# Performance work log

Measured on AMD Instinct MI355X. Metric: run time of the kernel, lower is better.

Reference implementation:

```python
import jax, jax.numpy as jnp
import numpy as np
import math

MODEL_DIM = 64
HEAD_DIM = 16


def setup_inputs() -> dict:
    key = jax.random.key(0)
    ks = jax.random.split(key, 9)
    B, T = 4, 4096
    idx = jax.random.normal(ks[0], (B, T, MODEL_DIM), dtype=jnp.float32)
    s_in = 1.0 / math.sqrt(MODEL_DIM)
    s_h = 1.0 / math.sqrt(HEAD_DIM)
    return {
        "idx": idx,
        "Wk": jax.random.normal(ks[1], (HEAD_DIM, MODEL_DIM), dtype=jnp.float32) * s_in,
        "bk": jax.random.normal(ks[2], (HEAD_DIM,), dtype=jnp.float32) * 0.02,
        "Wq": jax.random.normal(ks[3], (HEAD_DIM, MODEL_DIM), dtype=jnp.float32) * s_in,
        "bq": jax.random.normal(ks[4], (HEAD_DIM,), dtype=jnp.float32) * 0.02,
        "Wv": jax.random.normal(ks[5], (HEAD_DIM, MODEL_DIM), dtype=jnp.float32) * s_in,
        "bv": jax.random.normal(ks[6], (HEAD_DIM,), dtype=jnp.float32) * 0.02,
        "Wp": jax.random.normal(ks[7], (MODEL_DIM, HEAD_DIM), dtype=jnp.float32) * s_h,
        "bp": jax.random.normal(ks[8], (MODEL_DIM,), dtype=jnp.float32) * 0.02,
    }


def reference(idx, Wk, bk, Wq, bq, Wv, bv, Wp, bp):
    # idx: [B, T, model_dim]
    k = idx @ Wk.T + bk  # [B, T, H]
    q = idx @ Wq.T + bq
    v = idx @ Wv.T + bv
    scale = 1.0 / math.sqrt(HEAD_DIM)
    att = jnp.einsum("bth,bsh->bts", q, k) * scale  # [B, T, T]
    att = jnp.tril(att)
    # faithful to masked_fill(attention == 0, -inf): any exact-zero entry
    # (upper triangle after tril, plus accidental zeros) becomes -inf
    att = jnp.where(att == 0, -jnp.inf, att)
    att = jax.nn.softmax(att, axis=-1)
    av = jnp.einsum("bts,bsh->bth", att, v)  # [B, T, H]
    return av @ Wp.T + bp  # [B, T, model_dim]
```

## Files before the change

kernel.cpp:

```cpp
#include <hip/hip_runtime.h>
#include <hip/hip_bf16.h>
#include <stdint.h>

#define DEV __device__ __forceinline__

typedef short s4v __attribute__((ext_vector_type(4)));
typedef float f4v __attribute__((ext_vector_type(4)));

static constexpr int T = 4096;
static constexpr int BATCH = 4;
static constexpr int MD = 64;
static constexpr int H = 16;
static constexpr int PB = T * H;

#if __has_builtin(__builtin_amdgcn_mfma_f32_16x16x16bf16_1k)
DEV f4v mfma16(s4v a, s4v b, f4v c) {
    return __builtin_amdgcn_mfma_f32_16x16x16bf16_1k(a, b, c, 0, 0, 0);
}
#elif __has_builtin(__builtin_amdgcn_mfma_f32_16x16x16_bf16)
typedef __bf16 bf4v __attribute__((ext_vector_type(4)));
DEV f4v mfma16(s4v a, s4v b, f4v c) {
    return __builtin_amdgcn_mfma_f32_16x16x16_bf16(__builtin_bit_cast(bf4v, a),
                                                   __builtin_bit_cast(bf4v, b), c, 0, 0, 0);
}
#else
DEV f4v mfma16(s4v a, s4v b, f4v c) {
    asm("v_mfma_f32_16x16x16_bf16 %0, %1, %2, %0" : "+v"(c) : "v"(a), "v"(b));
    return c;
}
#endif

DEV short f2bf(float x) {
    uint32_t u = __builtin_bit_cast(uint32_t, x);
    u += 0x7fffu + ((u >> 16) & 1u);
    return (short)(u >> 16);
}

DEV float ex2(float x) {
#if __has_builtin(__builtin_amdgcn_exp2f)
    return __builtin_amdgcn_exp2f(x);
#else
    return exp2f(x);
#endif
}

__global__ __launch_bounds__(256) void k_proj(
    const float* __restrict__ idx,
    const float* __restrict__ Wk, const float* __restrict__ bk,
    const float* __restrict__ Wq, const float* __restrict__ bq,
    const float* __restrict__ Wv, const float* __restrict__ bv,
    short* __restrict__ qp, short* __restrict__ kp, short* __restrict__ vp)
{
    const int w = threadIdx.x >> 6, lane = threadIdx.x & 63;
    const int a = lane & 15, g = lane >> 4;
    const int tile = blockIdx.x * 4 + w;
    const int b = tile >> 8;
    const int trow0 = (tile & 255) << 4;

    const float* rb = idx + (size_t)(b * T + trow0) * MD;

    s4v xf[4], wqf[4], wkf[4], wvf[4];
#pragma unroll
    for (int kc = 0; kc < 4; ++kc) {
        const int ko = kc * 16 + 4 * g;
        f4v x = *(const f4v*)(rb + a * MD + ko);
        f4v q = *(const f4v*)(Wq + a * MD + ko);
        f4v k = *(const f4v*)(Wk + a * MD + ko);
        f4v v = *(const f4v*)(Wv + a * MD + ko);
        xf[kc]  = s4v{f2bf(x.x), f2bf(x.y), f2bf(x.z), f2bf(x.w)};
        wqf[kc] = s4v{f2bf(q.x), f2bf(q.y), f2bf(q.z), f2bf(q.w)};
        wkf[kc] = s4v{f2bf(k.x), f2bf(k.y), f2bf(k.z), f2bf(k.w)};
        wvf[kc] = s4v{f2bf(v.x), f2bf(v.y), f2bf(v.z), f2bf(v.w)};
    }
    f4v aq = {0.f,0.f,0.f,0.f}, ak = {0.f,0.f,0.f,0.f}, av = {0.f,0.f,0.f,0.f};
#pragma unroll
    for (int kc = 0; kc < 4; ++kc) {
        aq = mfma16(wqf[kc], xf[kc], aq);
        ak = mfma16(wkf[kc], xf[kc], ak);
        av = mfma16(xf[kc], wvf[kc], av);
    }
    const int slot = b * PB + (tile & 255) * 256 + g * 64 + a * 4;
    f4v bqv = *(const f4v*)(bq + 4 * g);
    f4v bkv = *(const f4v*)(bk + 4 * g);
    const float bvs = bv[a];
    const float CS = 0.36067376022224085f;
    *(s4v*)(qp + slot) = s4v{f2bf((aq.x + bqv.x) * CS), f2bf((aq.y + bqv.y) * CS),
                             f2bf((aq.z + bqv.z) * CS), f2bf((aq.w + bqv.w) * CS)};
    *(s4v*)(kp + slot) = s4v{f2bf(ak.x + bkv.x), f2bf(ak.y + bkv.y),
                             f2bf(ak.z + bkv.z), f2bf(ak.w + bkv.w)};
    *(s4v*)(vp + slot) = s4v{f2bf(av.x + bvs), f2bf(av.y + bvs),
                             f2bf(av.z + bvs), f2bf(av.w + bvs)};
}

DEV void proc_range(int lo, int hi, s4v Qf, int tq, int g,
                    const short* __restrict__ kb, const short* __restrict__ vb,
                    f4v& acc, float& lp)
{
    int st = lo;
    for (; st + 4 <= hi; st += 4) {
        s4v Kf[4], Vf[4];
#pragma unroll
        for (int u = 0; u < 4; ++u) {
            Kf[u] = *(const s4v*)(kb + (st + u) * 256);
            Vf[u] = *(const s4v*)(vb + (st + u) * 256);
        }
#pragma unroll
        for (int u = 0; u < 4; ++u) {
            f4v S = mfma16(Kf[u], Qf, f4v{0.f,0.f,0.f,0.f});
            const int sb = (st + u) * 16 + 4 * g;
            f4v p;
#pragma unroll
            for (int r = 0; r < 4; ++r) {
                const float e = ex2(S[r]);
                p[r] = (sb + r <= tq) ? e : 0.f;
            }
            lp += p.x + p.y + p.z + p.w;
            const s4v Pf = s4v{f2bf(p.x), f2bf(p.y), f2bf(p.z), f2bf(p.w)};
            acc = mfma16(Pf, Vf[u], acc);
        }
    }
    for (; st < hi; ++st) {
        s4v Kf = *(const s4v*)(kb + st * 256);
        s4v Vf = *(const s4v*)(vb + st * 256);
        f4v S = mfma16(Kf, Qf, f4v{0.f,0.f,0.f,0.f});
        const int sb = st * 16 + 4 * g;
        f4v p;
#pragma unroll
        for (int r = 0; r < 4; ++r) {
            const float e = ex2(S[r]);
            p[r] = (sb + r <= tq) ? e : 0.f;
        }
        lp += p.x + p.y + p.z + p.w;
        const s4v Pf = s4v{f2bf(p.x), f2bf(p.y), f2bf(p.z), f2bf(p.w)};
        acc = mfma16(Pf, Vf, acc);
    }
}

__global__ __launch_bounds__(256) void k_fused(
    const short* __restrict__ qp, const short* __restrict__ kp,
    const short* __restrict__ vp,
    const float* __restrict__ Wp, const float* __restrict__ bp,
    float* __restrict__ out)
{
    const int bx = blockIdx.x;
    const int b = bx >> 7, j = bx & 127;
    const int tid = threadIdx.x;
    const int w = tid >> 6, lane = tid & 63;
    const int a = lane & 15, g = lane >> 4;

    const int qtA = j, qtB = 255 - j;
    const int ntA = j + 1;
    const int ntot = 257;

    const short* qb = qp + b * PB;
    const short* kb = kp + b * PB + g * 64 + a * 4;
    const short* vb = vp + b * PB + g * 64 + a * 4;

    const s4v QfA = *(const s4v*)(qb + qtA * 256 + g * 64 + a * 4);
    const s4v QfB = *(const s4v*)(qb + qtB * 256 + g * 64 + a * 4);
    const int tqA = qtA * 16 + a, tqB = qtB * 16 + a;

    const int vLo = min(w * 65, ntot);
    const int vHi = min(vLo + 65, ntot);

    f4v accA = {0.f,0.f,0.f,0.f}, accB = {0.f,0.f,0.f,0.f};
    float lpA = 0.f, lpB = 0.f;

    proc_range(vLo, min(vHi, ntA), QfA, tqA, g, kb, vb, accA, lpA);
    proc_range(max(vLo - ntA, 0), vHi - ntA, QfB, tqB, g, kb, vb, accB, lpB);

    __shared__ float pacc[8 * 64 * 4];
    __shared__ float plp[8 * 16];

    *(f4v*)&pacc[((w * 2 + 0) * 64 + lane) * 4] = accA;
    *(f4v*)&pacc[((w * 2 + 1) * 64 + lane) * 4] = accB;

    float lA = lpA + __shfl_xor(lpA, 16); lA += __shfl_xor(lA, 32);
    float lB = lpB + __shfl_xor(lpB, 16); lB += __shfl_xor(lB, 32);
    if (lane < 16) {
        plp[(w * 2 + 0) * 16 + lane] = lA;
        plp[(w * 2 + 1) * 16 + lane] = lB;
    }
    __syncthreads();

    if (tid < 128) {
        const int X = tid >> 6, i = (tid >> 2) & 15, dc = tid & 3;
        float av[16];
#pragma unroll
        for (int h = 0; h < 16; ++h) av[h] = 0.f;
        float l = 0.f;
#pragma unroll
        for (int ww = 0; ww < 4; ++ww) {
            const int base = ((ww * 2 + X) * 64 + (i >> 2) * 16) * 4 + (i & 3);
#pragma unroll
            for (int h = 0; h < 16; ++h) av[h] += pacc[base + h * 4];
            l += plp[(ww * 2 + X) * 16 + i];
        }
        const float inv = 1.f / l;
        const int qt = X ? qtB : qtA;

        float* orow = out + ((size_t)(b * T) + qt * 16 + i) * 64 + dc * 16;
#pragma unroll
        for (int j4 = 0; j4 < 4; ++j4) {
            f4v o;
#pragma unroll
            for (int jj = 0; jj < 4; ++jj) {
                const int d = dc * 16 + j4 * 4 + jj;
                const float* wr = Wp + d * 16;
                float s = 0.f;
#pragma unroll
                for (int h = 0; h < 16; ++h) s += av[h] * wr[h];
                o[jj] = bp[d] + s * inv;
            }
            *(f4v*)(orow + j4 * 4) = o;
        }
    }
}

extern "C" void kernel_launch(void* const* d_in, const int* in_sizes, int n_in,
                              void* d_out, int out_size, void* d_ws, size_t ws_size,
                              hipStream_t stream) {
    const float* idx = (const float*)d_in[0];
    const float* Wk  = (const float*)d_in[1];
    const float* bk  = (const float*)d_in[2];
    const float* Wq  = (const float*)d_in[3];
    const float* bq  = (const float*)d_in[4];
    const float* Wv  = (const float*)d_in[5];
    const float* bv  = (const float*)d_in[6];
    const float* Wp  = (const float*)d_in[7];
    const float* bp  = (const float*)d_in[8];
    float* out = (float*)d_out;

    short* qp = (short*)d_ws;
    short* kp = qp + BATCH * PB;
    short* vp = kp + BATCH * PB;

    k_proj<<<256, 256, 0, stream>>>(idx, Wk, bk, Wq, bq, Wv, bv, qp, kp, vp);
    k_fused<<<512, 256, 0, stream>>>(qp, kp, vp, Wp, bp, out);
}
```

Measured before the change: 31.37 us.

## Double-buffer K/V register loads in groups of eight and mask only the final group

Rewrites the attention inner loop to process key tiles in groups of eight. The next group's K/V fragments are loaded into a second register set while the current group is computed, so global-load latency overlaps with MFMA and exp work. Causal masking now runs only in the last group of each range, since the diagonal tile always falls there. In exchange, register pressure rises with four arrays of eight fragments, which may reduce occupancy, and the tail loads clamp indices to valid tiles.

```diff
diff --git a/kernel.cpp b/kernel.cpp
--- a/kernel.cpp
+++ b/kernel.cpp
@@ -34,6 +34,10 @@
     uint32_t u = __builtin_bit_cast(uint32_t, x);
     u += 0x7fffu + ((u >> 16) & 1u);
     return (short)(u >> 16);
+}
+
+DEV s4v pack4(f4v p) {
+    return s4v{f2bf(p.x), f2bf(p.y), f2bf(p.z), f2bf(p.w)};
 }
 
 DEV float ex2(float x) {
@@ -67,10 +71,10 @@
         f4v q = *(const f4v*)(Wq + a * MD + ko);
         f4v k = *(const f4v*)(Wk + a * MD + ko);
         f4v v = *(const f4v*)(Wv + a * MD + ko);
-        xf[kc]  = s4v{f2bf(x.x), f2bf(x.y), f2bf(x.z), f2bf(x.w)};
-        wqf[kc] = s4v{f2bf(q.x), f2bf(q.y), f2bf(q.z), f2bf(q.w)};
-        wkf[kc] = s4v{f2bf(k.x), f2bf(k.y), f2bf(k.z), f2bf(k.w)};
-        wvf[kc] = s4v{f2bf(v.x), f2bf(v.y), f2bf(v.z), f2bf(v.w)};
+        xf[kc]  = pack4(x);
+        wqf[kc] = pack4(q);
+        wkf[kc] = pack4(k);
+        wvf[kc] = pack4(v);
     }
     f4v aq = {0.f,0.f,0.f,0.f}, ak = {0.f,0.f,0.f,0.f}, av = {0.f,0.f,0.f,0.f};
 #pragma unroll
@@ -84,56 +88,72 @@
     f4v bkv = *(const f4v*)(bk + 4 * g);
     const float bvs = bv[a];
     const float CS = 0.36067376022224085f;
-    *(s4v*)(qp + slot) = s4v{f2bf((aq.x + bqv.x) * CS), f2bf((aq.y + bqv.y) * CS),
-                             f2bf((aq.z + bqv.z) * CS), f2bf((aq.w + bqv.w) * CS)};
-    *(s4v*)(kp + slot) = s4v{f2bf(ak.x + bkv.x), f2bf(ak.y + bkv.y),
-                             f2bf(ak.z + bkv.z), f2bf(ak.w + bkv.w)};
-    *(s4v*)(vp + slot) = s4v{f2bf(av.x + bvs), f2bf(av.y + bvs),
-                             f2bf(av.z + bvs), f2bf(av.w + bvs)};
+    f4v qv = {(aq.x + bqv.x) * CS, (aq.y + bqv.y) * CS,
+              (aq.z + bqv.z) * CS, (aq.w + bqv.w) * CS};
+    f4v kv = {ak.x + bkv.x, ak.y + bkv.y, ak.z + bkv.z, ak.w + bkv.w};
+    f4v vv = {av.x + bvs, av.y + bvs, av.z + bvs, av.w + bvs};
+    *(s4v*)(qp + slot) = pack4(qv);
+    *(s4v*)(kp + slot) = pack4(kv);
+    *(s4v*)(vp + slot) = pack4(vv);
 }
 
 DEV void proc_range(int lo, int hi, s4v Qf, int tq, int g,
                     const short* __restrict__ kb, const short* __restrict__ vb,
                     f4v& acc, float& lp)
 {
-    int st = lo;
-    for (; st + 4 <= hi; st += 4) {
-        s4v Kf[4], Vf[4];
-#pragma unroll
-        for (int u = 0; u < 4; ++u) {
-            Kf[u] = *(const s4v*)(kb + (st + u) * 256);
-            Vf[u] = *(const s4v*)(vb + (st + u) * 256);
-        }
-#pragma unroll
-        for (int u = 0; u < 4; ++u) {
-            f4v S = mfma16(Kf[u], Qf, f4v{0.f,0.f,0.f,0.f});
-            const int sb = (st + u) * 16 + 4 * g;
-            f4v p;
-#pragma unroll
-            for (int r = 0; r < 4; ++r) {
-                const float e = ex2(S[r]);
-                p[r] = (sb + r <= tq) ? e : 0.f;
+    if (lo >= hi) return;
+    const int ng = (hi - lo + 7) >> 3;
+    s4v KA[8], VA[8], KB[8], VB[8];
+
+    auto LOADG = [&](s4v* K, s4v* V, int gi) {
+        const int st = lo + gi * 8;
+#pragma unroll
+        for (int u = 0; u < 8; ++u) {
+            const int idx = min(st + u, hi - 1);
+            K[u] = *(const s4v*)(kb + idx * 256);
+            V[u] = *(const s4v*)(vb + idx * 256);
+        }
+    };
+    auto COMPG = [&](const s4v* K, const s4v* V, int gi) {
+        const int st = lo + gi * 8;
+        if (gi == ng - 1) {
+#pragma unroll
+            for (int u = 0; u < 8; ++u) {
+                if (st + u < hi) {
+                    f4v S = mfma16(K[u], Qf, f4v{0.f,0.f,0.f,0.f});
+                    const int sb = (st + u) * 16 + 4 * g;
+                    f4v p;
+#pragma unroll
+                    for (int r = 0; r < 4; ++r) {
+                        const float e = ex2(S[r]);
+                        p[r] = (sb + r <= tq) ? e : 0.f;
+                    }
+                    lp += p.x + p.y + p.z + p.w;
+                    acc = mfma16(pack4(p), V[u], acc);
+                }
             }
-            lp += p.x + p.y + p.z + p.w;
-            const s4v Pf = s4v{f2bf(p.x), f2bf(p.y), f2bf(p.z), f2bf(p.w)};
-            acc = mfma16(Pf, Vf[u], acc);
-        }
-    }
-    for (; st < hi; ++st) {
-        s4v Kf = *(const s4v*)(kb + st * 256);
-        s4v Vf = *(const s4v*)(vb + st * 256);
-        f4v S = mfma16(Kf, Qf, f4v{0.f,0.f,0.f,0.f});
-        const int sb = st * 16 + 4 * g;
-        f4v p;
-#pragma unroll
-        for (int r = 0; r < 4; ++r) {
-            const float e = ex2(S[r]);
-            p[r] = (sb + r <= tq) ? e : 0.f;
-        }
-        lp += p.x + p.y + p.z + p.w;
-        const s4v Pf = s4v{f2bf(p.x), f2bf(p.y), f2bf(p.z), f2bf(p.w)};
-        acc = mfma16(Pf, Vf, acc);
-    }
+        } else {
+#pragma unroll
+            for (int u = 0; u < 8; ++u) {
+                f4v S = mfma16(K[u], Qf, f4v{0.f,0.f,0.f,0.f});
+                f4v p;
+#pragma unroll
+                for (int r = 0; r < 4; ++r) p[r] = ex2(S[r]);
+                lp += p.x + p.y + p.z + p.w;
+                acc = mfma16(pack4(p), V[u], acc);
+            }
+        }
+    };
+
+    int it = 0;
+    LOADG(KA, VA, 0);
+    for (; it + 2 <= ng; it += 2) {
+        LOADG(KB, VB, it + 1);
+        COMPG(KA, VA, it);
+        if (it + 2 < ng) LOADG(KA, VA, it + 2);
+        COMPG(KB, VB, it + 1);
+    }
+    if (it < ng) COMPG(KA, VA, it);
 }
 
 __global__ __launch_bounds__(256) void k_fused(
```

Result: no change. 31.12 us (-0.8%).
